# Optimization experiments

Measured on AMD Instinct MI355X. Metric: run time of the kernel, lower is better.

Reference implementation:

```python
import jax, jax.numpy as jnp
import numpy as np

N_P, N_W, F_IN = 512, 3584, 256
H1, O1 = 8, 32
H2, O2 = 8, 256
BATCH = 1024
NEG_SLOPE = 0.2


def _xavier(key, shape):
    fan_in, fan_out = shape[-2], shape[-1]
    lim = jnp.sqrt(6.0 / (fan_in + fan_out))
    return jax.random.uniform(key, shape, jnp.float32, -lim, lim)


def setup_inputs() -> dict:
    key = jax.random.key(0)
    ks = jax.random.split(key, 16)
    return {
        "input": jax.random.uniform(ks[0], (BATCH, N_W), jnp.float32),
        "pern_feature": jax.random.normal(ks[1], (N_P, F_IN), jnp.float32),
        "word_feature": jax.random.normal(ks[2], (N_W, F_IN), jnp.float32),
        "w1": _xavier(ks[3], (H1, F_IN, O1)),
        "a_src1": _xavier(ks[4], (H1, O1, 1)),
        "a_dst1": _xavier(ks[5], (H1, O1, 1)),
        "b1": jnp.zeros((O1,), jnp.float32),
        "w2": _xavier(ks[6], (H2, F_IN, O2)),
        "a_src2": _xavier(ks[7], (H2, F_IN, 1)),
        "a_dst2": _xavier(ks[8], (H2, F_IN, 1)),
        "b2": jnp.zeros((O2,), jnp.float32),
        "W_fc": _xavier(ks[9], (O2, 5)),
        "b_fc": jnp.zeros((5,), jnp.float32),
        "pern_adj": jax.random.randint(ks[10], (N_P, N_P), 0, 2, jnp.int32),
        "word_pern_adj": jax.random.randint(ks[11], (N_P + N_W, N_P + N_W), 0, 2, jnp.int32),
    }


def gat(h, adj, w, a_src, a_dst, bias):
    # h: [N, f_in], adj: [N, N] int, w: [H, f_in, f_out]
    h_prime = jnp.einsum('nf,hfo->hno', h, w)          # [H, N, O]
    t = jnp.tanh(h_prime)
    s_src = jnp.einsum('hno,hoi->hn', t, a_src)        # [H, N]
    s_dst = jnp.einsum('hno,hoi->hn', t, a_dst)        # [H, N]
    attn = s_src[:, :, None] + s_dst[:, None, :]       # [H, N, N]
    attn = jnp.where(attn >= 0, attn, NEG_SLOPE * attn)  # leaky_relu
    attn = jnp.where(adj[None, :, :] > 0, attn, -jnp.inf)
    attn = jax.nn.softmax(attn, axis=-1)
    out = jnp.einsum('hnm,hmo->hno', attn, h_prime)    # [H, N, O]
    return out + bias


def reference(input, pern_feature, word_feature, w1, a_src1, a_dst1, b1,
              w2, a_src2, a_dst2, b2, W_fc, b_fc, pern_adj, word_pern_adj):
    n_p = pern_feature.shape[0]
    # GAT 1 over personality graph
    h1 = gat(pern_feature, pern_adj, w1, a_src1, a_dst1, b1)       # [H1, n_p, O1]
    hiddn_pp = jnp.transpose(h1, (1, 0, 2)).reshape(n_p, -1)        # [n_p, H1*O1]
    hiddn_pp = jax.nn.elu(hiddn_pp)
    # dropout is identity in eval mode
    hiddn_wp = jnp.concatenate([word_feature, hiddn_pp], axis=0)    # [N, 256]
    h2 = gat(hiddn_wp, word_pern_adj, w2, a_src2, a_dst2, b2)       # [H2, N, O2]
    hiddn_wp2 = h2.mean(axis=0)                                     # [N, O2]
    hiddn_w = hiddn_wp2[:word_feature.shape[0], :]                  # [n_w, O2]
    x = (input @ hiddn_w) / input.sum(axis=1, keepdims=True)        # [B, O2]
    return x @ W_fc + b_fc                                          # [B, 5]
```

## Files before the change

kernel.cpp:

```cpp
#include <hip/hip_runtime.h>
#include <hip/hip_bf16.h>
#include <math.h>

#define NP 512
#define NW 3584
#define NT 4096
#define FIN 256
#define H1 8
#define O1 32
#define H2 8
#define O2 256
#define NEG 0.2f

typedef __attribute__((ext_vector_type(8))) short bf16x8;
typedef __attribute__((ext_vector_type(4))) float f32x4;
typedef __attribute__((ext_vector_type(2))) float v2f;
typedef unsigned long long u64;

__device__ __forceinline__ unsigned short f2bf(float f) {
    unsigned u = __float_as_uint(f);
    unsigned r = (u + 0x7FFF + ((u >> 16) & 1)) >> 16;
    return (unsigned short)r;
}

__device__ __forceinline__ float fast_tanh(float x) {
    float ex = __expf(2.0f * x);
    return 1.0f - 2.0f / (ex + 1.0f);
}

__global__ __launch_bounds__(256) void k_prep(
    const float* __restrict__ wf, const float* __restrict__ pf,
    const float* __restrict__ w1, const float* __restrict__ a_src1,
    const float* __restrict__ a_dst1, const float* __restrict__ w2,
    const float* __restrict__ b2, const float* __restrict__ W_fc,
    const int* __restrict__ wp_adj,
    unsigned short* __restrict__ abf, unsigned short* __restrict__ btbf,
    float* __restrict__ hp1, float* __restrict__ ss1, float* __restrict__ sd1,
    u64* __restrict__ maskT64, float* __restrict__ cvec)
{
    __shared__ float tile[64][65];
    __shared__ float feat[2][FIN];
    __shared__ float red[4][5];
    int blk = blockIdx.x;
    int t = threadIdx.x;
    if (blk < 896) {
        int idx4 = blk * 256 + t;
        float4 x = ((const float4*)wf)[idx4];
        ushort4 y;
        y.x = f2bf(x.x); y.y = f2bf(x.y); y.z = f2bf(x.z); y.w = f2bf(x.w);
        ((ushort4*)abf)[idx4] = y;
    } else if (blk < 1152) {
        int n0 = (blk - 896) * 2;
        feat[0][t] = pf[n0 * FIN + t];
        feat[1][t] = pf[(n0 + 1) * FIN + t];
        __syncthreads();
        int h = t >> 5, o = t & 31;
        float acc0 = 0.f, acc1 = 0.f;
        const float* wcol = w1 + h * FIN * O1 + o;
        #pragma unroll 4
        for (int f = 0; f < FIN; f++) {
            float w = wcol[f * O1];
            acc0 += feat[0][f] * w;
            acc1 += feat[1][f] * w;
        }
        hp1[n0 * 256 + t] = acc0;
        hp1[(n0 + 1) * 256 + t] = acc1;
        float as = a_src1[h * O1 + o];
        float ad = a_dst1[h * O1 + o];
        float accs[2] = {acc0, acc1};
        #pragma unroll
        for (int i = 0; i < 2; i++) {
            float th = tanhf(accs[i]);
            float vs = th * as, vd = th * ad;
            #pragma unroll
            for (int off = 1; off < 32; off <<= 1) {
                vs += __shfl_xor(vs, off);
                vd += __shfl_xor(vd, off);
            }
            if (o == 0) { ss1[h * NP + n0 + i] = vs; sd1[h * NP + n0 + i] = vd; }
        }
    } else if (blk < 1280) {
        int blk2 = blk - 1152;
        int h = blk2 >> 4;
        int f0 = ((blk2 >> 2) & 3) * 64;
        int o0 = (blk2 & 3) * 64;
        #pragma unroll
        for (int rr = 0; rr < 16; rr++) {
            int f = rr * 4 + (t >> 6);
            int o = t & 63;
            tile[f][o] = w2[((size_t)(h * FIN + f0 + f)) * O2 + o0 + o];
        }
        __syncthreads();
        #pragma unroll
        for (int rr = 0; rr < 16; rr++) {
            int o = rr * 4 + (t >> 6);
            int f = t & 63;
            btbf[((size_t)(h * O2 + o0 + o)) * FIN + f0 + f] = f2bf(tile[f][o]);
        }
    } else if (blk < 2176) {
        int w = t >> 6, l = t & 63;
        int r = (blk - 1280) * 4 + w;
        const int4* row = (const int4*)(wp_adj + (size_t)r * NT);
        for (int c4 = 0; c4 < 16; c4++) {
            int4 x = row[c4 * 64 + l];
            u64 nib = (u64)((x.x != 0 ? 1 : 0) | (x.y != 0 ? 2 : 0) |
                            (x.z != 0 ? 4 : 0) | (x.w != 0 ? 8 : 0));
            u64 v = nib << (4 * (l & 15));
            v |= __shfl_xor(v, 1);
            v |= __shfl_xor(v, 2);
            v |= __shfl_xor(v, 4);
            v |= __shfl_xor(v, 8);
            if ((l & 15) == 0) {
                int qw = c4 * 4 + (l >> 4);
                maskT64[(size_t)qw * NW + r] = v;
            }
        }
    } else {
        float v[5];
        #pragma unroll
        for (int j = 0; j < 5; j++) v[j] = b2[t] * W_fc[t * 5 + j];
        #pragma unroll
        for (int off = 1; off < 64; off <<= 1)
            #pragma unroll
            for (int j = 0; j < 5; j++) v[j] += __shfl_xor(v[j], off);
        int w = t >> 6, l = t & 63;
        if (l == 0) { for (int j = 0; j < 5; j++) red[w][j] = v[j]; }
        __syncthreads();
        if (t == 0)
            for (int j = 0; j < 5; j++) cvec[j] = red[0][j] + red[1][j] + red[2][j] + red[3][j];
    }
}

__global__ __launch_bounds__(256) void k_gat1_attn(
    const int* __restrict__ adj, const float* __restrict__ hp1,
    const float* __restrict__ ss1, const float* __restrict__ sd1,
    const float* __restrict__ b1, unsigned short* __restrict__ abf)
{
    __shared__ float p[2][H1][NP];
    __shared__ float den[2][H1];
    int t = threadIdx.x;
    int n0 = blockIdx.x * 2;
    for (int rr = 0; rr < 32; rr++) {
        int idx = rr * 256 + t;
        int i = idx >> 12, h = (idx >> 9) & 7, m = idx & 511;
        float a = adj[(n0 + i) * NP + m] > 0 ? 1.0f : 0.0f;
        float e = ss1[h * NP + n0 + i] + sd1[h * NP + m];
        e = fmaxf(e, NEG * e);
        p[i][h][m] = a * __expf(e);
    }
    __syncthreads();
    int w = t >> 6, l = t & 63;
    {
        int i = w & 1;
        #pragma unroll
        for (int hh = 0; hh < 4; hh++) {
            int h = (w >> 1) * 4 + hh;
            float s = 0;
            #pragma unroll
            for (int q = 0; q < 8; q++) s += p[i][h][l + 64 * q];
            #pragma unroll
            for (int off = 1; off < 64; off <<= 1) s += __shfl_xor(s, off);
            if (l == 0) den[i][h] = s;
        }
    }
    __syncthreads();
    int h = t >> 5, o = t & 31;
    float a0a = 0.f, a0b = 0.f, a1a = 0.f, a1b = 0.f;
    #pragma unroll 8
    for (int m = 0; m < NP; m += 2) {
        float v0 = hp1[m * 256 + t];
        float v1 = hp1[(m + 1) * 256 + t];
        a0a += p[0][h][m] * v0;
        a1a += p[1][h][m] * v0;
        a0b += p[0][h][m + 1] * v1;
        a1b += p[1][h][m + 1] * v1;
    }
    float acc[2] = {a0a + a0b, a1a + a1b};
    float bo = b1[o];
    #pragma unroll
    for (int i = 0; i < 2; i++) {
        float r = acc[i] / den[i][h] + bo;
        r = r > 0.f ? r : expm1f(r);
        abf[(NW + n0 + i) * FIN + t] = f2bf(r);
    }
}

__global__ __launch_bounds__(256) void k_gemm_hp2(
    const unsigned short* __restrict__ abf, const unsigned short* __restrict__ btbf,
    const float* __restrict__ a_src2, const float* __restrict__ a_dst2,
    const float* __restrict__ W_fc, float* __restrict__ gpart)
{
    __shared__ unsigned short As[128][264];
    int b = blockIdx.x;
    int nt = b & 1, h = (b >> 1) & 7, mt = b >> 4;
    int t = threadIdx.x;
    int w = t >> 6, l = t & 63;
    int m0 = mt * 128;
    {
        int row = t >> 5;
        int col8 = (t & 31) * 8;
        #pragma unroll
        for (int u = 0; u < 16; u++)
            *(bf16x8*)(&As[u * 8 + row][col8]) =
                *(const bf16x8*)(abf + (size_t)(m0 + u * 8 + row) * FIN + col8);
    }
    __syncthreads();
    int am0 = (w >> 1) * 64;
    int n0 = nt * 128 + (w & 1) * 64;
    int lr = l & 15, lq = l >> 4;
    const unsigned short* bbase = btbf + h * O2 * FIN;
    f32x4 acc[4][4];
    #pragma unroll
    for (int i = 0; i < 4; i++)
        #pragma unroll
        for (int j = 0; j < 4; j++) acc[i][j] = (f32x4){0.f, 0.f, 0.f, 0.f};
    #pragma unroll
    for (int k = 0; k < FIN; k += 32) {
        bf16x8 a[4], bf[4];
        int kc = k + lq * 8;
        #pragma unroll
        for (int j = 0; j < 4; j++)
            bf[j] = *(const bf16x8*)(bbase + (size_t)(n0 + j * 16 + lr) * FIN + kc);
        #pragma unroll
        for (int i = 0; i < 4; i++)
            a[i] = *(const bf16x8*)(&As[am0 + i * 16 + lr][kc]);
        #pragma unroll
        for (int i = 0; i < 4; i++)
            #pragma unroll
            for (int j = 0; j < 4; j++)
                acc[i][j] = __builtin_amdgcn_mfma_f32_16x16x32_bf16(a[i], bf[j], acc[i][j], 0, 0, 0);
    }
    int slice = nt * 2 + (w & 1);
    float as[4], ad[4], wfc[4][5];
    #pragma unroll
    for (int j = 0; j < 4; j++) {
        int col = n0 + j * 16 + lr;
        as[j] = a_src2[h * O2 + col];
        ad[j] = a_dst2[h * O2 + col];
        #pragma unroll
        for (int jj = 0; jj < 5; jj++) wfc[j][jj] = W_fc[col * 5 + jj];
    }
    float* base = gpart + ((size_t)h * 4 + slice) * NT * 8;
    #pragma unroll
    for (int i = 0; i < 4; i++) {
        #pragma unroll
        for (int r = 0; r < 4; r++) {
            float s[7] = {0,0,0,0,0,0,0};
            #pragma unroll
            for (int j = 0; j < 4; j++) {
                float x = acc[i][j][r];
                float th = fast_tanh(x);
                s[0] += th * as[j];
                s[1] += th * ad[j];
                #pragma unroll
                for (int jj = 0; jj < 5; jj++) s[2 + jj] += x * wfc[j][jj];
            }
            #pragma unroll
            for (int off = 1; off < 16; off <<= 1)
                #pragma unroll
                for (int q = 0; q < 7; q++) s[q] += __shfl_xor(s[q], off);
            if (lr == 0) {
                int m = m0 + am0 + i * 16 + lq * 4 + r;
                float* dst = base + (size_t)m * 8;
                #pragma unroll
                for (int q = 0; q < 7; q++) dst[q] = s[q];
            }
        }
    }
}

__global__ __launch_bounds__(256) void k_comb_hp2(
    const float* __restrict__ gpart,
    float* __restrict__ Etab, float* __restrict__ Eptab, float* __restrict__ T)
{
    int idx = blockIdx.x * 256 + threadIdx.x;
    float s[7] = {0,0,0,0,0,0,0};
    #pragma unroll
    for (int sl = 0; sl < 4; sl++) {
        const float* p = gpart + (((size_t)(idx >> 12) * 4 + sl) * NT + (idx & (NT - 1))) * 8;
        #pragma unroll
        for (int q = 0; q < 7; q++) s[q] += p[q];
    }
    Etab[idx]  = __expf(s[0]);
    Eptab[idx] = __expf(NEG * s[0]);
    float4 t0 = {__expf(s[1]), __expf(NEG * s[1]), 1.0f, s[2]};
    float4 t1 = {s[3], s[4], s[5], s[6]};
    *(float4*)(T + (size_t)idx * 8)     = t0;
    *(float4*)(T + (size_t)idx * 8 + 4) = t1;
}

__global__ __launch_bounds__(256) void k_gat2_attn(
    const u64* __restrict__ maskT64, const float* __restrict__ Etab,
    const float* __restrict__ Eptab, const float* __restrict__ T,
    float* __restrict__ part)
{
    int t = threadIdx.x;
    int w = t >> 6, l = t & 63;
    int b = blockIdx.x;
    int nb = b % 112;
    int h  = (b / 112) & 7;
    int c  = b / 896;
    int n0 = __builtin_amdgcn_readfirstlane(nb * 32 + w * 8);
    u64 epk[8];
    #pragma unroll
    for (int i = 0; i < 8; i++) {
        int r = h * NT + n0 + i;
        unsigned e  = __builtin_amdgcn_readfirstlane(__float_as_uint(Etab[r]));
        unsigned ep = __builtin_amdgcn_readfirstlane(__float_as_uint(Eptab[r]));
        epk[i] = ((u64)ep << 32) | e;
    }
    float den[8] = {0,0,0,0,0,0,0,0};
    float num[8][5] = {{0}};
    const float* Th = T + ((size_t)h * NT + c * 2048) * 8;
    for (int q = 0; q < 32; q++) {
        const float* tp = Th + (size_t)(q * 64 + l) * 8;
        f32x4 t0 = *(const f32x4*)tp;
        f32x4 t1 = *(const f32x4*)(tp + 4);
        v2f ffp = {t0.x, t0.y};
        size_t moff = (size_t)(c * 32 + q) * NW + n0;
        const u64* mq = maskT64 + moff;
        #pragma unroll
        for (int i = 0; i < 8; i++) {
            u64 wv = mq[i];
            unsigned wlo = __builtin_amdgcn_readfirstlane((unsigned)wv);
            unsigned whi = __builtin_amdgcn_readfirstlane((unsigned)(wv >> 32));
            u64 word = ((u64)whi << 32) | wlo;
            v2f pab;
            asm("v_pk_mul_f32 %0, %1, %2" : "=v"(pab) : "v"(ffp), "s"(epk[i]));
            float pp0 = fmaxf(pab.x, pab.y);
            float pp;
            asm("v_cndmask_b32 %0, 0, %1, %2" : "=v"(pp) : "v"(pp0), "s"(word));
            den[i] += pp;
            num[i][0] = fmaf(pp, t0.w, num[i][0]);
            num[i][1] = fmaf(pp, t1.x, num[i][1]);
            num[i][2] = fmaf(pp, t1.y, num[i][2]);
            num[i][3] = fmaf(pp, t1.z, num[i][3]);
            num[i][4] = fmaf(pp, t1.w, num[i][4]);
        }
    }
    #pragma unroll
    for (int i = 0; i < 8; i++) {
        float v[6];
        v[0] = den[i];
        #pragma unroll
        for (int j = 0; j < 5; j++) v[1 + j] = num[i][j];
        #pragma unroll
        for (int off = 1; off < 8; off <<= 1)
            #pragma unroll
            for (int k = 0; k < 6; k++) v[k] += __shfl_xor(v[k], off);
        if ((l & 7) == 0) {
            float* dst = part + ((((size_t)c * NW + n0 + i) * 8 + h) * 8 + (l >> 3)) * 8;
            #pragma unroll
            for (int k = 0; k < 6; k++) dst[k] = v[k];
        }
    }
}

__global__ __launch_bounds__(256) void k_gat2_comb(const float* __restrict__ part,
                                                   float* __restrict__ hf) {
    int idx = blockIdx.x * 256 + threadIdx.x;
    int n = idx >> 3, h = idx & 7;
    float den = 0, num[5] = {0,0,0,0,0};
    #pragma unroll
    for (int cc = 0; cc < 2; cc++) {
        #pragma unroll
        for (int s = 0; s < 8; s++) {
            const float* p = part + ((((size_t)cc * NW + n) * 8 + h) * 8 + s) * 8;
            float4 a = *(const float4*)p;
            float4 bq = *(const float4*)(p + 4);
            den += a.x;
            num[0] += a.y; num[1] += a.z; num[2] += a.w;
            num[3] += bq.x; num[4] += bq.y;
        }
    }
    float inv = 1.0f / (den * 8.0f);
    float v[5];
    #pragma unroll
    for (int j = 0; j < 5; j++) v[j] = num[j] * inv;
    #pragma unroll
    for (int off = 1; off < 8; off <<= 1)
        #pragma unroll
        for (int j = 0; j < 5; j++) v[j] += __shfl_xor(v[j], off);
    if (h == 0) {
        #pragma unroll
        for (int j = 0; j < 5; j++) hf[n * 5 + j] = v[j];
    }
}

__global__ __launch_bounds__(256) void k_final(
    const float* __restrict__ input, const float* __restrict__ hf,
    const float* __restrict__ cvec, const float* __restrict__ b_fc,
    float* __restrict__ out)
{
    int b = blockIdx.x, t = threadIdx.x;
    const float4* row4 = (const float4*)(input + (size_t)b * NW);
    const float4* hf4 = (const float4*)hf;
    float s = 0.f, a[5] = {0.f, 0.f, 0.f, 0.f, 0.f};
    for (int idx = t; idx < NW / 4; idx += 256) {
        float4 x = row4[idx];
        float f[20];
        #pragma unroll
        for (int q = 0; q < 5; q++) *(float4*)(f + 4 * q) = hf4[idx * 5 + q];
        s += x.x + x.y + x.z + x.w;
        #pragma unroll
        for (int j = 0; j < 5; j++)
            a[j] += x.x * f[j] + x.y * f[5 + j] + x.z * f[10 + j] + x.w * f[15 + j];
    }
    #pragma unroll
    for (int off = 1; off < 64; off <<= 1) {
        s += __shfl_xor(s, off);
        #pragma unroll
        for (int j = 0; j < 5; j++) a[j] += __shfl_xor(a[j], off);
    }
    __shared__ float red[4][6];
    int w = t >> 6, l = t & 63;
    if (l == 0) { red[w][0] = s; for (int j = 0; j < 5; j++) red[w][j + 1] = a[j]; }
    __syncthreads();
    if (t < 5) {
        float st = red[0][0] + red[1][0] + red[2][0] + red[3][0];
        float aj = red[0][t + 1] + red[1][t + 1] + red[2][t + 1] + red[3][t + 1];
        out[b * 5 + t] = aj / st + cvec[t] + b_fc[t];
    }
}

extern "C" void kernel_launch(void* const* d_in, const int* in_sizes, int n_in,
                              void* d_out, int out_size, void* d_ws, size_t ws_size,
                              hipStream_t stream) {
    const float* input   = (const float*)d_in[0];
    const float* pf      = (const float*)d_in[1];
    const float* wf      = (const float*)d_in[2];
    const float* w1      = (const float*)d_in[3];
    const float* a_src1  = (const float*)d_in[4];
    const float* a_dst1  = (const float*)d_in[5];
    const float* b1      = (const float*)d_in[6];
    const float* w2      = (const float*)d_in[7];
    const float* a_src2  = (const float*)d_in[8];
    const float* a_dst2  = (const float*)d_in[9];
    const float* b2      = (const float*)d_in[10];
    const float* W_fc    = (const float*)d_in[11];
    const float* b_fc    = (const float*)d_in[12];
    const int* pern_adj  = (const int*)d_in[13];
    const int* wp_adj    = (const int*)d_in[14];
    float* out = (float*)d_out;

    char* ws = (char*)d_ws;
    unsigned short* abf    = (unsigned short*)(ws);
    unsigned short* btbf   = (unsigned short*)(ws + 2097152);
    float*          hp1    = (float*)(ws + 3145728);
    float*          ss1    = (float*)(ws + 3670016);
    float*          sd1    = (float*)(ws + 3686400);
    float*          Etab   = (float*)(ws + 3833856);
    float*          Eptab  = (float*)(ws + 3964928);
    float*          T      = (float*)(ws + 4096000);
    float*          hf     = (float*)(ws + 5144576);
    float*          cvec   = (float*)(ws + 5216256);
    u64*            maskT64= (u64*)(ws + 5216512);
    float*          gpart  = (float*)(ws + 7051520);
    float*          part   = (float*)(ws + 11245824);

    k_prep<<<2177, 256, 0, stream>>>(wf, pf, w1, a_src1, a_dst1, w2, b2, W_fc,
                                     wp_adj, abf, btbf, hp1, ss1, sd1, maskT64, cvec);
    k_gat1_attn<<<256, 256, 0, stream>>>(pern_adj, hp1, ss1, sd1, b1, abf);
    k_gemm_hp2<<<512, 256, 0, stream>>>(abf, btbf, a_src2, a_dst2, W_fc, gpart);
    k_comb_hp2<<<128, 256, 0, stream>>>(gpart, Etab, Eptab, T);
    k_gat2_attn<<<1792, 256, 0, stream>>>(maskT64, Etab, Eptab, T, part);
    k_gat2_comb<<<112, 256, 0, stream>>>(part, hf);
    k_final<<<1024, 256, 0, stream>>>(input, hf, cvec, b_fc, out);
}
```

Baseline: 239.9 us.

## Split hp2 GEMM epilogue into separate bf16-transposed store and reduction kernel

Removes the tanh, attention-score and W_fc projection epilogue from the MFMA GEMM kernel. The GEMM now writes the full hp2 per head as transposed bf16 to workspace, and a new k_reduce kernel reads it back column by column to compute the seven per-node partial sums. The aim is to drop the heavy cross-lane shuffle reduction and register pressure from the GEMM. In exchange it adds a large intermediate tensor that must be written and reread, uses narrow strided stores from the GEMM, and rounds hp2 to bf16 before tanh and the projection. The new buffer also shares its workspace offset with the `part` buffer.

```diff
diff --git a/kernel.cpp b/kernel.cpp
--- a/kernel.cpp
+++ b/kernel.cpp
@@ -22,10 +22,8 @@
     unsigned r = (u + 0x7FFF + ((u >> 16) & 1)) >> 16;
     return (unsigned short)r;
 }
-
-__device__ __forceinline__ float fast_tanh(float x) {
-    float ex = __expf(2.0f * x);
-    return 1.0f - 2.0f / (ex + 1.0f);
+__device__ __forceinline__ float bf2f(unsigned short s) {
+    return __uint_as_float(((unsigned)s) << 16);
 }
 
 __global__ __launch_bounds__(256) void k_prep(
@@ -187,26 +185,24 @@
 
 __global__ __launch_bounds__(256) void k_gemm_hp2(
     const unsigned short* __restrict__ abf, const unsigned short* __restrict__ btbf,
-    const float* __restrict__ a_src2, const float* __restrict__ a_dst2,
-    const float* __restrict__ W_fc, float* __restrict__ gpart)
-{
-    __shared__ unsigned short As[128][264];
+    unsigned short* __restrict__ hp2T)
+{
+    __shared__ unsigned short As[64][264];
     int b = blockIdx.x;
-    int nt = b & 1, h = (b >> 1) & 7, mt = b >> 4;
+    int h = b & 7, mt = b >> 3;
     int t = threadIdx.x;
     int w = t >> 6, l = t & 63;
-    int m0 = mt * 128;
+    int m0 = mt * 64;
     {
         int row = t >> 5;
         int col8 = (t & 31) * 8;
         #pragma unroll
-        for (int u = 0; u < 16; u++)
+        for (int u = 0; u < 8; u++)
             *(bf16x8*)(&As[u * 8 + row][col8]) =
                 *(const bf16x8*)(abf + (size_t)(m0 + u * 8 + row) * FIN + col8);
     }
     __syncthreads();
-    int am0 = (w >> 1) * 64;
-    int n0 = nt * 128 + (w & 1) * 64;
+    int n0 = w * 64;
     int lr = l & 15, lq = l >> 4;
     const unsigned short* bbase = btbf + h * O2 * FIN;
     f32x4 acc[4][4];
@@ -223,50 +219,50 @@
             bf[j] = *(const bf16x8*)(bbase + (size_t)(n0 + j * 16 + lr) * FIN + kc);
         #pragma unroll
         for (int i = 0; i < 4; i++)
-            a[i] = *(const bf16x8*)(&As[am0 + i * 16 + lr][kc]);
+            a[i] = *(const bf16x8*)(&As[i * 16 + lr][kc]);
         #pragma unroll
         for (int i = 0; i < 4; i++)
             #pragma unroll
             for (int j = 0; j < 4; j++)
-                acc[i][j] = __builtin_amdgcn_mfma_f32_16x16x32_bf16(a[i], bf[j], acc[i][j], 0, 0, 0);
-    }
-    int slice = nt * 2 + (w & 1);
-    float as[4], ad[4], wfc[4][5];
-    #pragma unroll
-    for (int j = 0; j < 4; j++) {
-        int col = n0 + j * 16 + lr;
-        as[j] = a_src2[h * O2 + col];
-        ad[j] = a_dst2[h * O2 + col];
-        #pragma unroll
-        for (int jj = 0; jj < 5; jj++) wfc[j][jj] = W_fc[col * 5 + jj];
-    }
-    float* base = gpart + ((size_t)h * 4 + slice) * NT * 8;
-    #pragma unroll
-    for (int i = 0; i < 4; i++) {
-        #pragma unroll
-        for (int r = 0; r < 4; r++) {
-            float s[7] = {0,0,0,0,0,0,0};
-            #pragma unroll
-            for (int j = 0; j < 4; j++) {
-                float x = acc[i][j][r];
-                float th = fast_tanh(x);
-                s[0] += th * as[j];
-                s[1] += th * ad[j];
-                #pragma unroll
-                for (int jj = 0; jj < 5; jj++) s[2 + jj] += x * wfc[j][jj];
+                acc[i][j] = __builtin_amdgcn_mfma_f32_16x16x32_bf16(bf[j], a[i], acc[i][j], 0, 0, 0);
+    }
+    #pragma unroll
+    for (int i = 0; i < 4; i++)
+        #pragma unroll
+        for (int j = 0; j < 4; j++)
+            #pragma unroll
+            for (int r = 0; r < 4; r++) {
+                int o = n0 + j * 16 + lq * 4 + r;
+                hp2T[((size_t)h * O2 + o) * NT + m0 + i * 16 + lr] = f2bf(acc[i][j][r]);
             }
-            #pragma unroll
-            for (int off = 1; off < 16; off <<= 1)
-                #pragma unroll
-                for (int q = 0; q < 7; q++) s[q] += __shfl_xor(s[q], off);
-            if (lr == 0) {
-                int m = m0 + am0 + i * 16 + lq * 4 + r;
-                float* dst = base + (size_t)m * 8;
-                #pragma unroll
-                for (int q = 0; q < 7; q++) dst[q] = s[q];
-            }
-        }
-    }
+}
+
+__global__ __launch_bounds__(256) void k_reduce(
+    const unsigned short* __restrict__ hp2T,
+    const float* __restrict__ a_src2, const float* __restrict__ a_dst2,
+    const float* __restrict__ W_fc, float* __restrict__ gpart)
+{
+    int b = blockIdx.x;
+    int cs = b & 3, mb = (b >> 2) & 15, h = b >> 6;
+    int m = mb * 256 + threadIdx.x;
+    float s[7] = {0,0,0,0,0,0,0};
+    const unsigned short* base = hp2T + ((size_t)h * O2 + cs * 64) * NT + m;
+    #pragma unroll 8
+    for (int oi = 0; oi < 64; oi++) {
+        int o = cs * 64 + oi;
+        float x = bf2f(base[(size_t)oi * NT]);
+        float ex = __expf(2.0f * x);
+        float th = 1.0f - 2.0f * __builtin_amdgcn_rcpf(ex + 1.0f);
+        s[0] += th * a_src2[h * O2 + o];
+        s[1] += th * a_dst2[h * O2 + o];
+        #pragma unroll
+        for (int jj = 0; jj < 5; jj++) s[2 + jj] += x * W_fc[o * 5 + jj];
+    }
+    float* dst = gpart + (((size_t)(h * 4 + cs)) * NT + m) * 8;
+    float4 d0 = {s[0], s[1], s[2], s[3]};
+    float4 d1 = {s[4], s[5], s[6], 0.f};
+    *(float4*)dst = d0;
+    *(float4*)(dst + 4) = d1;
 }
 
 __global__ __launch_bounds__(256) void k_comb_hp2(
@@ -456,12 +452,14 @@
     float*          cvec   = (float*)(ws + 5216256);
     u64*            maskT64= (u64*)(ws + 5216512);
     float*          gpart  = (float*)(ws + 7051520);
+    unsigned short* hp2T   = (unsigned short*)(ws + 11245824);
     float*          part   = (float*)(ws + 11245824);
 
     k_prep<<<2177, 256, 0, stream>>>(wf, pf, w1, a_src1, a_dst1, w2, b2, W_fc,
                                      wp_adj, abf, btbf, hp1, ss1, sd1, maskT64, cvec);
     k_gat1_attn<<<256, 256, 0, stream>>>(pern_adj, hp1, ss1, sd1, b1, abf);
-    k_gemm_hp2<<<512, 256, 0, stream>>>(abf, btbf, a_src2, a_dst2, W_fc, gpart);
+    k_gemm_hp2<<<512, 256, 0, stream>>>(abf, btbf, hp2T);
+    k_reduce<<<512, 256, 0, stream>>>(hp2T, a_src2, a_dst2, W_fc, gpart);
     k_comb_hp2<<<128, 256, 0, stream>>>(gpart, Etab, Eptab, T);
     k_gat2_attn<<<1792, 256, 0, stream>>>(maskT64, Etab, Eptab, T, part);
     k_gat2_comb<<<112, 256, 0, stream>>>(part, hf);
```

After: 250.7 us. +4.5%, slower.
